# Optimization experiments

Hardware: AMD Instinct MI355X
Metric: run time of the kernel (lower is better)

## Reference

```python
import jax, jax.numpy as jnp
import numpy as np


def grid_sample_bilinear_border(img, grid):
    """Faithful F.grid_sample(mode='bilinear', padding_mode='border', align_corners=True).
    img: (B, C, H, W), grid: (B, P, Q, 2) with (x, y) in [-1, 1]. Returns (B, C, P, Q)."""
    B, C, H, W = img.shape
    gx = (grid[..., 0] + 1.0) * 0.5 * (W - 1)  # (B,P,Q) unnormalized x
    gy = (grid[..., 1] + 1.0) * 0.5 * (H - 1)
    # border padding: clamp coordinates into the image
    gx = jnp.clip(gx, 0.0, W - 1)
    gy = jnp.clip(gy, 0.0, H - 1)
    x0f = jnp.floor(gx)
    y0f = jnp.floor(gy)
    wx1 = gx - x0f
    wy1 = gy - y0f
    x0 = x0f.astype(jnp.int32)
    y0 = y0f.astype(jnp.int32)
    x1 = jnp.clip(x0 + 1, 0, W - 1)
    y1 = jnp.clip(y0 + 1, 0, H - 1)

    def sample_one(imgb, yi, xi):  # imgb (C,H,W); yi,xi (P,Q) -> (C,P,Q)
        return imgb[:, yi, xi]

    gather = jax.vmap(sample_one)
    v00 = gather(img, y0, x0)
    v01 = gather(img, y0, x1)
    v10 = gather(img, y1, x0)
    v11 = gather(img, y1, x1)
    wx1 = wx1[:, None]  # (B,1,P,Q) broadcast over C
    wy1 = wy1[:, None]
    wx0 = 1.0 - wx1
    wy0 = 1.0 - wy1
    return (v00 * wy0 * wx0 + v01 * wy0 * wx1 + v10 * wy1 * wx0 + v11 * wy1 * wx1)


def setup_inputs() -> dict:
    key = jax.random.key(0)
    k1, k2, k3, k4 = jax.random.split(key, 4)
    B, C, H, W, N = 2, 128, 800, 640, 10000
    image_features = jax.random.normal(k1, (B, C, H, W), dtype=jnp.float32)
    # normalized coords in [-1, 1]
    vertices = jax.random.uniform(k2, (B, N, 2), dtype=jnp.float32, minval=-1.0, maxval=1.0)
    conv_w = jax.random.normal(k3, (18, C), dtype=jnp.float32) * 0.02
    conv_b = jax.random.normal(k4, (18,), dtype=jnp.float32) * 0.02
    return {"image_features": image_features, "vertices": vertices,
            "conv_w": conv_w, "conv_b": conv_b}


def reference(image_features, vertices, conv_w, conv_b):
    B, N, _ = vertices.shape
    # 1) sample features at the vertex centers: grid (B,N,1,2) -> (B,C,N)
    center = vertices[:, :, None, :]
    feats = grid_sample_bilinear_border(image_features, center)[:, :, :, 0]  # (B,C,N)
    # 2) 1x1 conv predicting 9 (x,y) offsets per vertex
    delta = jnp.einsum('bcn,oc->bon', feats, conv_w) + conv_b[None, :, None]  # (B,18,N)
    delta = delta.transpose(0, 2, 1).reshape(B, N, 9, 2)
    delta = delta.at[:, :, 0, :].set(0.0)  # first neighbour is the center itself
    # 3) sample 9 neighbours per vertex and mean-pool
    neigh = vertices[:, :, None, :] + delta  # (B,N,9,2)
    nfeat = grid_sample_bilinear_border(image_features, neigh)  # (B,C,N,9)
    out = jnp.mean(nfeat, axis=-1)  # (B,C,N)
    return out.transpose(0, 2, 1)  # (B,N,C)
```

## Files before the change

kernel.cpp:

```cpp
#include <hip/hip_runtime.h>

constexpr int BB = 2;
constexpr int CC = 128;
constexpr int HH = 800;
constexpr int WW = 640;
constexpr int NN = 10000;
constexpr int OO = 18;
constexpr int NP = BB * NN;
constexpr size_t HWsz = (size_t)HH * WW;
constexpr int TP = 64;
constexpr int TILES_PER_B = (int)(HWsz / TP);
constexpr size_t WS_TRANS_BYTES = (size_t)BB * HWsz * CC * sizeof(float);

constexpr int S2 = NP * 8;
constexpr int BAND_SHIFT = 2;
constexpr int NB = (HH + (1 << BAND_SHIFT) - 1) >> BAND_SHIFT;
constexpr size_t WS_COORDS = 0;
constexpr size_t WS_SGX    = WS_COORDS + sizeof(float) * 2 * S2;
constexpr size_t WS_SGY    = WS_SGX + sizeof(float) * S2;
constexpr size_t WS_SID    = WS_SGY + sizeof(float) * S2;
constexpr size_t WS_HIST   = WS_SID + sizeof(unsigned) * S2;
constexpr size_t WS_CUR    = WS_HIST + sizeof(unsigned) * 256;
constexpr size_t WS_BAND_NEEDED = WS_CUR + sizeof(unsigned) * 256;

__device__ __forceinline__ float to_px_x(float v) {
    float g = (v + 1.0f) * 0.5f * (float)(WW - 1);
    return fminf(fmaxf(g, 0.0f), (float)(WW - 1));
}
__device__ __forceinline__ float to_px_y(float v) {
    float g = (v + 1.0f) * 0.5f * (float)(HH - 1);
    return fminf(fmaxf(g, 0.0f), (float)(HH - 1));
}


__global__ void __launch_bounds__(256)
kT(const float* __restrict__ img, float* __restrict__ trans) {
    __shared__ float lds[CC][TP + 1];
    const int tile = blockIdx.x;
    const int b = tile / TILES_PER_B;
    const int pix0 = (tile - b * TILES_PER_B) * TP;

    const int cg   = threadIdx.x & 15;
    const int crow = threadIdx.x >> 4;
    #pragma unroll
    for (int r = 0; r < 8; ++r) {
        const int c = r * 16 + crow;
        const float4 v = *(const float4*)(img + ((size_t)(b * CC + c)) * HWsz + pix0 + 4 * cg);
        lds[c][4 * cg + 0] = v.x;
        lds[c][4 * cg + 1] = v.y;
        lds[c][4 * cg + 2] = v.z;
        lds[c][4 * cg + 3] = v.w;
    }
    __syncthreads();

    const int c2    = threadIdx.x & 127;
    const int phalf = threadIdx.x >> 7;
    float* tbase = trans + ((size_t)b * HWsz + pix0) * CC;
    #pragma unroll 4
    for (int w = 0; w < 32; ++w) {
        const int pix = w * 2 + phalf;
        tbase[(size_t)pix * CC + c2] = lds[c2][pix];
    }
}

__device__ __forceinline__ float bilin_nhwc(const float* __restrict__ tb,
                                            float gx, float gy, int c) {
    float x0f = floorf(gx);
    float y0f = floorf(gy);
    int x0 = (int)x0f;
    int y0 = (int)y0f;
    int x1 = min(x0 + 1, WW - 1);
    int y1 = min(y0 + 1, HH - 1);
    float wx1 = gx - x0f;
    float wy1 = gy - y0f;
    float wx0 = 1.0f - wx1;
    float wy0 = 1.0f - wy1;
    const float* r0 = tb + (size_t)y0 * WW * CC;
    const float* r1 = tb + (size_t)y1 * WW * CC;
    float v00 = r0[(size_t)x0 * CC + c];
    float v01 = r0[(size_t)x1 * CC + c];
    float v10 = r1[(size_t)x0 * CC + c];
    float v11 = r1[(size_t)x1 * CC + c];
    return (v00 * wx0 + v01 * wx1) * wy0 + (v10 * wx0 + v11 * wx1) * wy1;
}

__global__ void __launch_bounds__(CC)
kG(const float* __restrict__ trans, const float* __restrict__ verts,
   const float* __restrict__ conv_w, const float* __restrict__ conv_b,
   float* __restrict__ out) {
    const int p = blockIdx.x;
    const int b = p / NN;
    const int c = threadIdx.x;

    __shared__ float s_feat[CC];
    __shared__ float s_delta[OO];

    const float vx = verts[(size_t)p * 2 + 0];
    const float vy = verts[(size_t)p * 2 + 1];
    const float* tb = trans + (size_t)b * HWsz * CC;

    const float fc = bilin_nhwc(tb, to_px_x(vx), to_px_y(vy), c);
    s_feat[c] = fc;
    __syncthreads();

    if (c < OO) {
        float acc = conv_b[c];
        const float* wrow = conv_w + c * CC;
        #pragma unroll 8
        for (int k = 0; k < CC; ++k) acc += wrow[k] * s_feat[k];
        s_delta[c] = acc;
    }
    __syncthreads();

    float acc = fc;
    #pragma unroll
    for (int j = 1; j < 9; ++j) {
        const float nx = vx + s_delta[2 * j + 0];
        const float ny = vy + s_delta[2 * j + 1];
        acc += bilin_nhwc(tb, to_px_x(nx), to_px_y(ny), c);
    }
    out[(size_t)p * CC + c] = acc * (1.0f / 9.0f);
}


__device__ __forceinline__ float bilin_px(const float* __restrict__ base,
                                          float gx, float gy) {
    float x0f = floorf(gx);
    float y0f = floorf(gy);
    int x0 = (int)x0f;
    int y0 = (int)y0f;
    int x1 = min(x0 + 1, WW - 1);
    int y1 = min(y0 + 1, HH - 1);
    float wx1 = gx - x0f;
    float wy1 = gy - y0f;
    float wx0 = 1.0f - wx1;
    float wy0 = 1.0f - wy1;
    const float* r0 = base + (size_t)y0 * WW;
    const float* r1 = base + (size_t)y1 * WW;
    return (r0[x0] * wx0 + r0[x1] * wx1) * wy0 +
           (r1[x0] * wx0 + r1[x1] * wx1) * wy1;
}

__global__ void __launch_bounds__(CC)
k1_center(const float* __restrict__ img, const float* __restrict__ verts,
          const float* __restrict__ conv_w, const float* __restrict__ conv_b,
          float* __restrict__ out, float2* __restrict__ coords,
          unsigned* __restrict__ hist) {
    const int p = blockIdx.x;
    const int b = p / NN;
    const int c = threadIdx.x;
    __shared__ float s_feat[CC];
    __shared__ float s_delta[OO];
    const float vx = verts[(size_t)p * 2 + 0];
    const float vy = verts[(size_t)p * 2 + 1];
    const float* base = img + ((size_t)(b * CC + c)) * HWsz;
    const float fc = bilin_px(base, to_px_x(vx), to_px_y(vy));
    s_feat[c] = fc;
    __syncthreads();
    if (c < OO) {
        float acc = conv_b[c];
        const float* wrow = conv_w + c * CC;
        for (int k = 0; k < CC; ++k) acc += wrow[k] * s_feat[k];
        s_delta[c] = acc;
    }
    __syncthreads();
    out[(size_t)p * CC + c] = fc * (1.0f / 9.0f);
    if (c >= 1 && c < 9) {
        const float ggx = to_px_x(vx + s_delta[2 * c + 0]);
        const float ggy = to_px_y(vy + s_delta[2 * c + 1]);
        coords[p * 8 + (c - 1)] = make_float2(ggx, ggy);
        atomicAdd(&hist[((int)ggy) >> BAND_SHIFT], 1u);
    }
}

__global__ void k2_scan(const unsigned* __restrict__ hist, unsigned* __restrict__ cursor) {
    if (threadIdx.x == 0 && blockIdx.x == 0) {
        unsigned acc = 0;
        for (int i = 0; i < NB; ++i) { cursor[i] = acc; acc += hist[i]; }
    }
}

__global__ void __launch_bounds__(256)
k3_scatter(const float2* __restrict__ coords, unsigned* __restrict__ cursor,
           float* __restrict__ sgx, float* __restrict__ sgy, unsigned* __restrict__ sid) {
    const int i = blockIdx.x * 256 + threadIdx.x;
    if (i < S2) {
        const float2 cd = coords[i];
        const unsigned pos = atomicAdd(&cursor[((int)cd.y) >> BAND_SHIFT], 1u);
        sgx[pos] = cd.x; sgy[pos] = cd.y; sid[pos] = (unsigned)(i >> 3);
    }
}

__global__ void __launch_bounds__(CC)
k4_sample(const float* __restrict__ img, const float* __restrict__ sgx,
          const float* __restrict__ sgy, const unsigned* __restrict__ sid,
          float* __restrict__ out) {
    const int r = blockIdx.x;
    const int c = threadIdx.x;
    const unsigned p = sid[r];
    const int b = (p >= (unsigned)NN) ? 1 : 0;
    const float* base = img + ((size_t)(b * CC + c)) * HWsz;
    const float v = bilin_px(base, sgx[r], sgy[r]);
    atomicAdd(&out[(size_t)p * CC + c], v * (1.0f / 9.0f));
}


__global__ void __launch_bounds__(CC)
lns_kernel(const float* __restrict__ img, const float* __restrict__ verts,
           const float* __restrict__ conv_w, const float* __restrict__ conv_b,
           float* __restrict__ out) {
    const int p = blockIdx.x;
    const int b = p / NN;
    const int c = threadIdx.x;
    __shared__ float s_feat[CC];
    __shared__ float s_delta[OO];
    const float vx = verts[(size_t)p * 2 + 0];
    const float vy = verts[(size_t)p * 2 + 1];
    const float* base = img + ((size_t)(b * CC + c)) * HWsz;
    const float fc = bilin_px(base, to_px_x(vx), to_px_y(vy));
    s_feat[c] = fc;
    __syncthreads();
    if (c < OO) {
        float acc = conv_b[c];
        const float* wrow = conv_w + c * CC;
        for (int k = 0; k < CC; ++k) acc += wrow[k] * s_feat[k];
        s_delta[c] = acc;
    }
    __syncthreads();
    float acc = fc;
    for (int j = 1; j < 9; ++j)
        acc += bilin_px(base, to_px_x(vx + s_delta[2 * j]), to_px_y(vy + s_delta[2 * j + 1]));
    out[(size_t)p * CC + c] = acc * (1.0f / 9.0f);
}

extern "C" void kernel_launch(void* const* d_in, const int* in_sizes, int n_in,
                              void* d_out, int out_size, void* d_ws, size_t ws_size,
                              hipStream_t stream) {
    const float* img    = (const float*)d_in[0];
    const float* verts  = (const float*)d_in[1];
    const float* conv_w = (const float*)d_in[2];
    const float* conv_b = (const float*)d_in[3];
    float* out = (float*)d_out;

    if (ws_size >= WS_TRANS_BYTES) {
        float* trans = (float*)d_ws;
        kT<<<dim3(BB * TILES_PER_B), dim3(256), 0, stream>>>(img, trans);
        kG<<<dim3(NP), dim3(CC), 0, stream>>>(trans, verts, conv_w, conv_b, out);
        return;
    }

    if (ws_size >= WS_BAND_NEEDED) {
        char* w = (char*)d_ws;
        float2*   coords = (float2*)(w + WS_COORDS);
        float*    sgx    = (float*)(w + WS_SGX);
        float*    sgy    = (float*)(w + WS_SGY);
        unsigned* sid    = (unsigned*)(w + WS_SID);
        unsigned* hist   = (unsigned*)(w + WS_HIST);
        unsigned* cursor = (unsigned*)(w + WS_CUR);
        hipMemsetAsync(hist, 0, sizeof(unsigned) * 256, stream);
        k1_center<<<dim3(NP), dim3(CC), 0, stream>>>(img, verts, conv_w, conv_b, out, coords, hist);
        k2_scan<<<dim3(1), dim3(64), 0, stream>>>(hist, cursor);
        k3_scatter<<<dim3((S2 + 255) / 256), dim3(256), 0, stream>>>(coords, cursor, sgx, sgy, sid);
        k4_sample<<<dim3(S2), dim3(CC), 0, stream>>>(img, sgx, sgy, sid, out);
        return;
    }

    lns_kernel<<<dim3(NP), dim3(CC), 0, stream>>>(img, verts, conv_w, conv_b, out);
}
```

Measured before the change: 838.4 us.

## Vectorize NCHW-to-NHWC transpose stores and pack eight points per gather block

The transpose kernel now stores its LDS tile pixel-major and writes float4 rows to global memory instead of scalar stores. The gather kernel handles eight vertices per 256-thread block, with 32 lanes per vertex each loading float4 channel slices, and the 1x1 conv is spread across 144 threads. This targets memory instruction count and per-block overhead in both kernels. The transpose's LDS reads may now have more bank conflicts, and block-level syncs now span eight points.

```diff
diff --git a/kernel.cpp b/kernel.cpp
--- a/kernel.cpp
+++ b/kernel.cpp
@@ -35,36 +35,42 @@
 
 __global__ void __launch_bounds__(256)
 kT(const float* __restrict__ img, float* __restrict__ trans) {
-    __shared__ float lds[CC][TP + 1];
+    __shared__ float lds[TP][CC + 1];
     const int tile = blockIdx.x;
     const int b = tile / TILES_PER_B;
     const int pix0 = (tile - b * TILES_PER_B) * TP;
-
-    const int cg   = threadIdx.x & 15;
-    const int crow = threadIdx.x >> 4;
+    const int t = threadIdx.x;
+
+    const int cg   = t & 15;
+    const int crow = t >> 4;
     #pragma unroll
     for (int r = 0; r < 8; ++r) {
         const int c = r * 16 + crow;
         const float4 v = *(const float4*)(img + ((size_t)(b * CC + c)) * HWsz + pix0 + 4 * cg);
-        lds[c][4 * cg + 0] = v.x;
-        lds[c][4 * cg + 1] = v.y;
-        lds[c][4 * cg + 2] = v.z;
-        lds[c][4 * cg + 3] = v.w;
-    }
-    __syncthreads();
-
-    const int c2    = threadIdx.x & 127;
-    const int phalf = threadIdx.x >> 7;
+        lds[4 * cg + 0][c] = v.x;
+        lds[4 * cg + 1][c] = v.y;
+        lds[4 * cg + 2][c] = v.z;
+        lds[4 * cg + 3][c] = v.w;
+    }
+    __syncthreads();
+
+    const int pl = t & 7;
+    const int k  = t >> 3;
     float* tbase = trans + ((size_t)b * HWsz + pix0) * CC;
-    #pragma unroll 4
-    for (int w = 0; w < 32; ++w) {
-        const int pix = w * 2 + phalf;
-        tbase[(size_t)pix * CC + c2] = lds[c2][pix];
-    }
-}
-
-__device__ __forceinline__ float bilin_nhwc(const float* __restrict__ tb,
-                                            float gx, float gy, int c) {
+    #pragma unroll
+    for (int it = 0; it < 8; ++it) {
+        const int pix = it * 8 + pl;
+        float4 v;
+        v.x = lds[pix][4 * k + 0];
+        v.y = lds[pix][4 * k + 1];
+        v.z = lds[pix][4 * k + 2];
+        v.w = lds[pix][4 * k + 3];
+        *(float4*)(tbase + (size_t)pix * CC + 4 * k) = v;
+    }
+}
+
+__device__ __forceinline__ float4 bilin4(const float* __restrict__ tb,
+                                         float gx, float gy, int c4) {
     float x0f = floorf(gx);
     float y0f = floorf(gy);
     int x0 = (int)x0f;
@@ -75,51 +81,69 @@
     float wy1 = gy - y0f;
     float wx0 = 1.0f - wx1;
     float wy0 = 1.0f - wy1;
-    const float* r0 = tb + (size_t)y0 * WW * CC;
-    const float* r1 = tb + (size_t)y1 * WW * CC;
-    float v00 = r0[(size_t)x0 * CC + c];
-    float v01 = r0[(size_t)x1 * CC + c];
-    float v10 = r1[(size_t)x0 * CC + c];
-    float v11 = r1[(size_t)x1 * CC + c];
-    return (v00 * wx0 + v01 * wx1) * wy0 + (v10 * wx0 + v11 * wx1) * wy1;
-}
-
-__global__ void __launch_bounds__(CC)
+    const float* r0 = tb + ((size_t)y0 * WW) * CC;
+    const float* r1 = tb + ((size_t)y1 * WW) * CC;
+    const float4 v00 = *(const float4*)(r0 + (size_t)x0 * CC + c4);
+    const float4 v01 = *(const float4*)(r0 + (size_t)x1 * CC + c4);
+    const float4 v10 = *(const float4*)(r1 + (size_t)x0 * CC + c4);
+    const float4 v11 = *(const float4*)(r1 + (size_t)x1 * CC + c4);
+    float4 r;
+    r.x = (v00.x * wx0 + v01.x * wx1) * wy0 + (v10.x * wx0 + v11.x * wx1) * wy1;
+    r.y = (v00.y * wx0 + v01.y * wx1) * wy0 + (v10.y * wx0 + v11.y * wx1) * wy1;
+    r.z = (v00.z * wx0 + v01.z * wx1) * wy0 + (v10.z * wx0 + v11.z * wx1) * wy1;
+    r.w = (v00.w * wx0 + v01.w * wx1) * wy0 + (v10.w * wx0 + v11.w * wx1) * wy1;
+    return r;
+}
+
+constexpr int PPB = 8;
+__global__ void __launch_bounds__(256)
 kG(const float* __restrict__ trans, const float* __restrict__ verts,
    const float* __restrict__ conv_w, const float* __restrict__ conv_b,
    float* __restrict__ out) {
-    const int p = blockIdx.x;
-    const int b = p / NN;
-    const int c = threadIdx.x;
-
-    __shared__ float s_feat[CC];
-    __shared__ float s_delta[OO];
+    const int t    = threadIdx.x;
+    const int pt   = t >> 5;
+    const int lane = t & 31;
+    const int c4   = lane * 4;
+    const int p    = blockIdx.x * PPB + pt;
+    const int b    = p / NN;
+
+    __shared__ float s_feat[PPB][CC + 4];
+    __shared__ float s_delta[PPB][OO];
 
     const float vx = verts[(size_t)p * 2 + 0];
     const float vy = verts[(size_t)p * 2 + 1];
     const float* tb = trans + (size_t)b * HWsz * CC;
 
-    const float fc = bilin_nhwc(tb, to_px_x(vx), to_px_y(vy), c);
-    s_feat[c] = fc;
-    __syncthreads();
-
-    if (c < OO) {
-        float acc = conv_b[c];
-        const float* wrow = conv_w + c * CC;
+    const float4 fc = bilin4(tb, to_px_x(vx), to_px_y(vy), c4);
+    s_feat[pt][c4 + 0] = fc.x;
+    s_feat[pt][c4 + 1] = fc.y;
+    s_feat[pt][c4 + 2] = fc.z;
+    s_feat[pt][c4 + 3] = fc.w;
+    __syncthreads();
+
+    if (t < PPB * OO) {
+        const int pp = t / OO;
+        const int o  = t - pp * OO;
+        float acc = conv_b[o];
+        const float* wrow = conv_w + o * CC;
         #pragma unroll 8
-        for (int k = 0; k < CC; ++k) acc += wrow[k] * s_feat[k];
-        s_delta[c] = acc;
-    }
-    __syncthreads();
-
-    float acc = fc;
+        for (int kk = 0; kk < CC; ++kk) acc += wrow[kk] * s_feat[pp][kk];
+        s_delta[pp][o] = acc;
+    }
+    __syncthreads();
+
+    float4 acc = fc;
     #pragma unroll
     for (int j = 1; j < 9; ++j) {
-        const float nx = vx + s_delta[2 * j + 0];
-        const float ny = vy + s_delta[2 * j + 1];
-        acc += bilin_nhwc(tb, to_px_x(nx), to_px_y(ny), c);
-    }
-    out[(size_t)p * CC + c] = acc * (1.0f / 9.0f);
+        const float nx = vx + s_delta[pt][2 * j + 0];
+        const float ny = vy + s_delta[pt][2 * j + 1];
+        const float4 v = bilin4(tb, to_px_x(nx), to_px_y(ny), c4);
+        acc.x += v.x; acc.y += v.y; acc.z += v.z; acc.w += v.w;
+    }
+    const float s = 1.0f / 9.0f;
+    float4 res;
+    res.x = acc.x * s; res.y = acc.y * s; res.z = acc.z * s; res.w = acc.w * s;
+    *(float4*)(out + (size_t)p * CC + c4) = res;
 }
 
 
@@ -245,7 +269,7 @@
     if (ws_size >= WS_TRANS_BYTES) {
         float* trans = (float*)d_ws;
         kT<<<dim3(BB * TILES_PER_B), dim3(256), 0, stream>>>(img, trans);
-        kG<<<dim3(NP), dim3(CC), 0, stream>>>(trans, verts, conv_w, conv_b, out);
+        kG<<<dim3(NP / PPB), dim3(256), 0, stream>>>(trans, verts, conv_w, conv_b, out);
         return;
     }
 
```

New measurement: 833.7 us. No clear change (-0.6%).
